# Optimization experiments

Hardware: AMD Instinct MI355X
Metric: run time of the kernel (lower is better)

The kernel has to match this reference:

```python
import math
import jax, jax.numpy as jnp
import numpy as np

HIDDEN = 2048
N_HEAD = 16
HEAD_DIM = HIDDEN // N_HEAD
LAYER_NUMBER = 1  # max(1, layer_number)
NORM_FACTOR = math.sqrt(HEAD_DIM) * LAYER_NUMBER


def build_alibi(seq_len, n_head):
    # n_head is a power of 2 -> slopes_i = 2^(-8*(i+1)/n_head)  (ALiBi paper)
    slopes = 2.0 ** (-8.0 * jnp.arange(1, n_head + 1, dtype=jnp.float32) / n_head)
    pos = jnp.arange(seq_len, dtype=jnp.float32)
    return slopes[:, None, None] * pos[None, None, :]  # (n_head, 1, seq_len)


def setup_inputs() -> dict:
    key = jax.random.key(0)
    ks = jax.random.split(key, 6)
    B, S = 2, 2048
    hidden_states = jax.random.normal(ks[0], (B, S, HIDDEN), jnp.float32)
    residual = jax.random.normal(ks[1], (B, S, HIDDEN), jnp.float32)
    attention_mask = jnp.ones((B, S), jnp.float32)  # no padding
    W_qkv = jax.random.normal(ks[2], (3 * HIDDEN, HIDDEN), jnp.float32) * (1.0 / math.sqrt(HIDDEN))
    b_qkv = jax.random.normal(ks[3], (3 * HIDDEN,), jnp.float32) * 0.02
    W_dense = jax.random.normal(ks[4], (HIDDEN, HIDDEN), jnp.float32) * (1.0 / math.sqrt(HIDDEN))
    b_dense = jax.random.normal(ks[5], (HIDDEN,), jnp.float32) * 0.02
    return {"hidden_states": hidden_states, "residual": residual,
            "attention_mask": attention_mask, "W_qkv": W_qkv, "b_qkv": b_qkv,
            "W_dense": W_dense, "b_dense": b_dense}


def reference(hidden_states, residual, attention_mask, W_qkv, b_qkv, W_dense, b_dense):
    B, S, H = hidden_states.shape
    nh, hd = N_HEAD, HEAD_DIM

    # fused QKV projection; split_tensor_along_last_dim over the per-head 3*hd axis
    mixed = hidden_states @ W_qkv.T + b_qkv              # [B,S,3H]
    mixed = mixed.reshape(B, S, nh, 3, hd)
    q = mixed[..., 0, :]                                  # [B,S,nh,hd]
    k = mixed[..., 1, :]
    v = mixed[..., 2, :]

    # baddbmm: beta*alibi + alpha*(q @ k^T)
    alibi = build_alibi(S, nh)                            # (nh,1,S)
    beta = 1.0 / LAYER_NUMBER
    alpha = 1.0 / NORM_FACTOR
    scores = alpha * jnp.einsum('bqnd,bknd->bnqk', q, k) + beta * alibi[None]  # [B,nh,S,S]

    # BloomScaledSoftmax: scale by layer_number, apply padded causal mask,
    # softmax in fp32, zero out masked probs
    scores = scores * LAYER_NUMBER
    mask_bool = attention_mask == 0.0                     # [B,S] True where padded
    causal = jnp.tril(jnp.ones((S, S), dtype=bool))       # [S,S]
    padded = (mask_bool[:, None, :, None]                 # query side
              | (~causal)[None, None]                     # causal
              | mask_bool[:, None, None, :])              # key side -> [B,1,S,S]
    scores = jnp.where(padded, jnp.float32(-10000.0), scores)
    probs = jax.nn.softmax(scores.astype(jnp.float32), axis=-1) * (~padded)
    probs = probs.astype(v.dtype)

    # attention_dropout/hidden_dropout are identity in eval mode
    context = jnp.einsum('bnqk,bknd->bqnd', probs, v).reshape(B, S, H)
    out = context @ W_dense.T + b_dense                   # dense (skip_bias_add folded)
    return residual + out
```

## Files before the change

### kernel.cpp

```cpp
#include <hip/hip_runtime.h>
#include <math.h>

#define HIDDEN 2048
#define NHEAD 16
#define HD 128
#define SEQ 2048
#define BATCH 2
#define MROWS (BATCH * SEQ)
#define K3 (3 * HIDDEN)

#define SCORE_SCALE 0.08838834764831845f

using short8 = __attribute__((ext_vector_type(8))) short;
using f32x4 = __attribute__((ext_vector_type(4))) float;

__device__ __forceinline__ unsigned short f2bf(float f) {
  union { float f; unsigned int u; } v; v.f = f;
  const unsigned int u = v.u;
  return (unsigned short)((u + 0x7FFFu + ((u >> 16) & 1u)) >> 16);
}

__device__ __forceinline__ void gl2lds16(const void* g, void* l) {
#pragma clang diagnostic push
#pragma clang diagnostic ignored "-Waddress-space-conversion"
  __builtin_amdgcn_global_load_lds(
      (const __attribute__((address_space(1))) unsigned int*)g,
      (__attribute__((address_space(3))) unsigned int*)l, 16, 0, 0);
#pragma clang diagnostic pop
}

template <int N>
__device__ __forceinline__ void vmwait() {
  asm volatile("s_waitcnt vmcnt(%0)" ::"n"(N) : "memory");
}

template <int V> struct IC { static constexpr int v = V; };
template <bool V> struct BC { static constexpr bool v = V; };

__global__ __launch_bounds__(256) void cvt_all(
    const float* __restrict__ s0, unsigned short* __restrict__ d0, int n0,
    const float* __restrict__ s1, unsigned short* __restrict__ d1, int n1,
    const float* __restrict__ s2, unsigned short* __restrict__ d2, int n2) {
  int i = (blockIdx.x * 256 + threadIdx.x) * 8;
  const float* src;
  unsigned short* dst;
  if (i < n0) {
    src = s0; dst = d0;
  } else if (i < n0 + n1) {
    src = s1; dst = d1; i -= n0;
  } else {
    src = s2; dst = d2; i -= n0 + n1;
    if (i >= n2) return;
  }
  const float4 a = *(const float4*)(src + i);
  const float4 b = *(const float4*)(src + i + 4);
  ushort4 oa, ob;
  oa.x = f2bf(a.x); oa.y = f2bf(a.y); oa.z = f2bf(a.z); oa.w = f2bf(a.w);
  ob.x = f2bf(b.x); ob.y = f2bf(b.y); ob.z = f2bf(b.z); ob.w = f2bf(b.w);
  *(ushort4*)(dst + i) = oa;
  *(ushort4*)(dst + i + 4) = ob;
}

template <int MODE, int BROWS>
__global__ __launch_bounds__(512, 2) void gemm256(
    const unsigned short* __restrict__ A, const unsigned short* __restrict__ W,
    const float* __restrict__ bias, const float* __restrict__ residual,
    unsigned short* __restrict__ q, unsigned short* __restrict__ k,
    unsigned short* __restrict__ v, float* __restrict__ outf) {
  constexpr int K = HIDDEN;
  constexpr int NT = K / 64;
  constexpr int NB = BROWS / 64;
  constexpr int ABUF = 32768;
  constexpr int AUNIT = 16384;
  constexpr int BTB = BROWS * 128;
  constexpr int BUNIT = BTB / 2;
  constexpr int LA = 2;
  constexpr int LB = BROWS / 128;
  constexpr int WA = LA + LB;
  __shared__ __align__(16) unsigned short L[(2 * ABUF + 2 * BTB) / 2];

  const int tid = threadIdx.x;
  const int lane = tid & 63;
  const int l15 = lane & 15;
  const int quad = (lane >> 4) & 3;
  const int wave = tid >> 6;
  const int wr = wave >> 2;
  const int wc = wave & 3;

  const int gx = gridDim.x;
  const int nwg = gx * gridDim.y;
  const int flat = blockIdx.y * gx + blockIdx.x;
  const int swz = (flat & 7) * (nwg >> 3) + (flat >> 3);
  const int bx = swz % gx, by = swz / gx;
  const int n0 = bx * BROWS;
  const int m0 = by << 8;

  f32x4 acc[8][NB];
#pragma unroll
  for (int i = 0; i < 8; ++i)
#pragma unroll
    for (int j = 0; j < NB; ++j) {
      f32x4 z = {0.f, 0.f, 0.f, 0.f};
      acc[i][j] = z;
    }

  auto stageAk = [&](const int t, const int buf, const int kk) {
#pragma unroll
    for (int p = 0; p < LA; ++p) {
      const int idx = tid + p * 512;
      gl2lds16(A + (size_t)(m0 + (idx & 255)) * K + t * 64 + kk * 32 +
                   (idx >> 8) * 8,
               (char*)L + buf * ABUF + kk * AUNIT + idx * 16);
    }
  };
  auto stageBk = [&](const int t, const int buf, const int kk) {
#pragma unroll
    for (int p = 0; p < LB; ++p) {
      const int idx = tid + p * 512;
      gl2lds16(W + (size_t)(n0 + (idx & (BROWS - 1))) * K + t * 64 + kk * 32 +
                   (idx / BROWS) * 8,
               (char*)L + 2 * ABUF + buf * BTB + kk * BUNIT + idx * 16);
    }
  };

  short8 afA[4], afB[4], bf0[NB], bf1[NB];

  auto readA = [&](short8 (&dst)[4], const char* lA, const int kk,
                   const int mh) {
#pragma unroll
    for (int i = 0; i < 4; ++i)
      dst[i] = *(const short8*)(
          lA + kk * AUNIT +
          ((quad * 256 + wr * 128 + mh * 64 + i * 16 + l15) << 4));
  };
  auto readB = [&](short8 (&dst)[NB], const char* lB, const int kk) {
#pragma unroll
    for (int j = 0; j < NB; ++j)
      dst[j] = *(const short8*)(
          lB + kk * BUNIT +
          ((quad * BROWS + wc * (BROWS / 4) + j * 16 + l15) << 4));
  };
  auto mfmaC = [&](auto mhc, short8 (&af)[4], short8 (&bf)[NB]) {
    constexpr int MH = decltype(mhc)::v;
    __builtin_amdgcn_s_setprio(1);
#pragma unroll
    for (int i = 0; i < 4; ++i)
#pragma unroll
      for (int j = 0; j < NB; ++j)
        acc[MH + i][j] = __builtin_amdgcn_mfma_f32_16x16x32_bf16(
            af[i], bf[j], acc[MH + i][j], 0, 0, 0);
    __builtin_amdgcn_s_setprio(0);
    __builtin_amdgcn_sched_barrier(0);
  };

  auto tile = [&](const int c, const int t, auto s1c, auto s0c, auto r0c,
                  auto wac, auto wbc) {
    constexpr bool S1 = decltype(s1c)::v;
    constexpr bool S0 = decltype(s0c)::v;
    constexpr bool R0 = decltype(r0c)::v;
    const char* lA = (const char*)L + c * ABUF;
    const char* lB = (const char*)L + 2 * ABUF + c * BTB;
    const char* lAn = (const char*)L + (c ^ 1) * ABUF;
    const char* lBn = (const char*)L + 2 * ABUF + (c ^ 1) * BTB;
    vmwait<decltype(wac)::v>();
    __builtin_amdgcn_s_barrier();
    readA(afB, lA, 1, 0);
    readB(bf1, lB, 1);
    if (S1) stageAk(t + 1, c ^ 1, 1);
    __builtin_amdgcn_sched_barrier(0);
    mfmaC(IC<0>{}, afA, bf0);
    readA(afA, lA, 0, 1);
    if (S1) stageBk(t + 1, c ^ 1, 1);
    __builtin_amdgcn_sched_barrier(0);
    mfmaC(IC<0>{}, afB, bf1);
    readA(afB, lA, 1, 1);
    __builtin_amdgcn_sched_barrier(0);
    mfmaC(IC<4>{}, afA, bf0);
    vmwait<decltype(wbc)::v>();
    __builtin_amdgcn_s_barrier();
    if (R0) {
      readA(afA, lAn, 0, 0);
      readB(bf0, lBn, 0);
    }
    if (S0) {
      stageAk(t + 2, c, 0);
      stageBk(t + 2, c, 0);
    }
    __builtin_amdgcn_sched_barrier(0);
    mfmaC(IC<4>{}, afB, bf1);
  };

  stageAk(0, 0, 0);
  stageBk(0, 0, 0);
  stageAk(0, 0, 1);
  stageBk(0, 0, 1);
  stageAk(1, 1, 0);
  stageBk(1, 1, 0);
  vmwait<2 * WA>();
  __builtin_amdgcn_s_barrier();
  readA(afA, (const char*)L, 0, 0);
  readB(bf0, (const char*)L + 2 * ABUF, 0);

#pragma unroll 1
  for (int t = 0; t < NT - 2; ++t)
    tile(t & 1, t, BC<true>{}, BC<true>{}, BC<true>{}, IC<WA>{}, IC<WA>{});
  tile((NT - 2) & 1, NT - 2, BC<true>{}, BC<false>{}, BC<true>{}, IC<WA>{},
       IC<WA>{});
  tile((NT - 1) & 1, NT - 1, BC<false>{}, BC<false>{}, BC<false>{}, IC<0>{},
       IC<0>{});

  if (MODE == 0) {
#pragma unroll
    for (int mi = 0; mi < 8; ++mi) {
#pragma unroll
      for (int nj = 0; nj < NB; ++nj) {
        const int n = n0 + wc * (BROWS / 4) + nj * 16 + l15;
        const float bi = bias[n];
        const int h = n / 384;
        const int rem = n - h * 384;
        const int which = rem >> 7;
        const int d = rem & 127;
        const int mb = m0 + wr * 128 + mi * 16 + quad * 4;
        const int bb = mb >> 11, ssb = mb & 2047;
        const int bh = (bb << 4) + h;
        if (which == 2) {
          const int dt = d >> 4, dl = d & 15;
          const int ksup = ssb >> 5, ntl = (ssb >> 4) & 1, qq = (ssb >> 2) & 3;
          ushort4 pk;
          pk.x = f2bf(acc[mi][nj][0] + bi);
          pk.y = f2bf(acc[mi][nj][1] + bi);
          pk.z = f2bf(acc[mi][nj][2] + bi);
          pk.w = f2bf(acc[mi][nj][3] + bi);
          *(ushort4*)(v +
                      ((((size_t)(bh * 8 + dt) * (SEQ / 32) + ksup) * 4 + qq) *
                       16 + dl) * 8 + ntl * 4) = pk;
        } else {
          unsigned short* dst = (which == 0) ? q : k;
#pragma unroll
          for (int p = 0; p < 4; ++p)
            dst[((size_t)(bh << 11) + ssb + p) * HD + d] =
                f2bf(acc[mi][nj][p] + bi);
        }
      }
    }
  } else {
#pragma unroll
    for (int mi = 0; mi < 8; ++mi) {
#pragma unroll
      for (int nj = 0; nj < NB; ++nj) {
        const int n = n0 + wc * (BROWS / 4) + nj * 16 + l15;
        const float bi = bias[n];
#pragma unroll
        for (int p = 0; p < 4; ++p) {
          const int m = m0 + wr * 128 + mi * 16 + quad * 4 + p;
          outf[(size_t)m * HIDDEN + n] =
              acc[mi][nj][p] + bi + residual[(size_t)m * HIDDEN + n];
        }
      }
    }
  }
}

__global__ __launch_bounds__(256) void attn_mfma3(
    const unsigned short* __restrict__ qb, const unsigned short* __restrict__ kb,
    const unsigned short* __restrict__ vt4, unsigned short* __restrict__ ctx) {
  __shared__ __align__(16) unsigned short Ks[8192];
  __shared__ __align__(16) unsigned short Vs[8192];

  const int tid = threadIdx.x;
  const int lane = tid & 63;
  const int w = tid >> 6;
  const int l15 = lane & 15;
  const int quad = lane >> 4;
  const int bt = gridDim.x - 1 - blockIdx.x;
  const int q0 = bt << 6;
  const int h = blockIdx.y, b = blockIdx.z;
  const int bh = b * NHEAD + h;
  const float slope = exp2f(-0.5f * (float)(h + 1));
  const unsigned short* qp = qb + ((size_t)bh * SEQ + q0 + w * 16) * HD;
  const unsigned short* kp = kb + (size_t)bh * SEQ * HD;
  const unsigned short* vp = vt4 + (size_t)bh * SEQ * HD;

  short8 qf[4];
#pragma unroll
  for (int dt = 0; dt < 4; ++dt)
    qf[dt] = *(const short8*)(qp + (size_t)l15 * HD + dt * 32 + quad * 8);

  f32x4 O[8];
#pragma unroll
  for (int i = 0; i < 8; ++i) {
    f32x4 z = {0.f, 0.f, 0.f, 0.f};
    O[i] = z;
  }
  float mrow = -3.0e38f, lrow = 0.f;
  const int qg = q0 + w * 16 + l15;

  for (int kt = 0; kt <= bt; ++kt) {
#pragma unroll
    for (int p = 0; p < 4; ++p) {
      const int idx = tid + p * 256;
      const int reg = idx >> 6;
      const int nts = reg >> 2, dts = reg & 3;
      const int qs = (idx >> 4) & 3, ls = idx & 15;
      gl2lds16(kp + (size_t)(kt * 64 + nts * 16 + ls) * HD + dts * 32 + qs * 8,
               (char*)Ks + idx * 16);
    }
#pragma unroll
    for (int p = 0; p < 4; ++p) {
      const int idx = tid + p * 256;
      const int ntv = idx >> 7, off = idx & 127;
      gl2lds16(vp + ((size_t)(ntv * 64 + kt * 2)) * 512 + off * 8,
               (char*)Vs + idx * 16);
    }
    __syncthreads();

    f32x4 sc[4];
#pragma unroll
    for (int nt = 0; nt < 4; ++nt) {
      f32x4 z = {0.f, 0.f, 0.f, 0.f};
      sc[nt] = z;
    }
    const int ntmax = (kt == bt) ? (w + 1) : 4;
#pragma unroll
    for (int dt = 0; dt < 4; ++dt) {
#pragma unroll
      for (int nt = 0; nt < 4; ++nt) {
        if (nt < ntmax) {
          const short8 kf = *(const short8*)(
              (const char*)Ks + ((((nt * 4 + dt) * 4 + quad) * 16 + l15) << 4));
          sc[nt] = __builtin_amdgcn_mfma_f32_16x16x32_bf16(kf, qf[dt], sc[nt],
                                                           0, 0, 0);
        }
      }
    }

    const bool diag = (kt == bt);
    float pv[4][4];
    float pm = -3.0e38f;
#pragma unroll
    for (int nt = 0; nt < 4; ++nt) {
      const int kbase = kt * 64 + nt * 16 + quad * 4;
#pragma unroll
      for (int r = 0; r < 4; ++r) {
        const int kg = kbase + r;
        float s = fmaf(sc[nt][r], SCORE_SCALE, slope * (float)kg);
        if (diag && kg > qg) s = -1.0e30f;
        pv[nt][r] = s;
        pm = fmaxf(pm, s);
      }
    }
    pm = fmaxf(pm, __shfl_xor(pm, 16, 64));
    pm = fmaxf(pm, __shfl_xor(pm, 32, 64));
    const float mnew = fmaxf(mrow, pm);
    const float alpha = __expf(mrow - mnew);
    mrow = mnew;
    float rsum = 0.f;
#pragma unroll
    for (int nt = 0; nt < 4; ++nt)
#pragma unroll
      for (int r = 0; r < 4; ++r) {
        const float p = __expf(pv[nt][r] - mnew);
        pv[nt][r] = p;
        rsum += p;
      }
    rsum += __shfl_xor(rsum, 16, 64);
    rsum += __shfl_xor(rsum, 32, 64);
    lrow = lrow * alpha + rsum;

    float aO[4];
#pragma unroll
    for (int r = 0; r < 4; ++r)
      aO[r] = __shfl(alpha, (quad << 4) + (quad << 2) + r, 64);
#pragma unroll
    for (int o = 0; o < 8; ++o)
#pragma unroll
      for (int r = 0; r < 4; ++r) O[o][r] *= aO[r];

    union { short8 s; unsigned int u[4]; } pf[2];
#pragma unroll
    for (int nt = 0; nt < 4; ++nt) {
      const unsigned int lo =
          (unsigned int)f2bf(pv[nt][0]) | ((unsigned int)f2bf(pv[nt][1]) << 16);
      const unsigned int hi =
          (unsigned int)f2bf(pv[nt][2]) | ((unsigned int)f2bf(pv[nt][3]) << 16);
      pf[nt >> 1].u[(nt & 1) * 2] = lo;
      pf[nt >> 1].u[(nt & 1) * 2 + 1] = hi;
    }

#pragma unroll
    for (int s2 = 0; s2 < 2; ++s2) {
#pragma unroll
      for (int nt = 0; nt < 8; ++nt) {
        const short8 vf = *(const short8*)(
            (const char*)Vs + nt * 2048 + s2 * 1024 + quad * 256 + l15 * 16);
        O[nt] = __builtin_amdgcn_mfma_f32_16x16x32_bf16(pf[s2].s, vf, O[nt],
                                                        0, 0, 0);
      }
    }
    __syncthreads();
  }

  const float linv = 1.f / lrow;
  float iO[4];
#pragma unroll
  for (int r = 0; r < 4; ++r)
    iO[r] = __shfl(linv, (quad << 4) + (quad << 2) + r, 64);
#pragma unroll
  for (int nt = 0; nt < 8; ++nt)
#pragma unroll
    for (int r = 0; r < 4; ++r)
      ctx[((size_t)b * SEQ + q0 + w * 16 + quad * 4 + r) * HIDDEN + h * HD +
          nt * 16 + l15] = f2bf(O[nt][r] * iO[r]);
}

extern "C" void kernel_launch(void* const* d_in, const int* in_sizes, int n_in,
                              void* d_out, int out_size, void* d_ws,
                              size_t ws_size, hipStream_t stream) {
  const float* hs = (const float*)d_in[0];
  const float* res = (const float*)d_in[1];
  const float* Wqkv = (const float*)d_in[3];
  const float* bqkv = (const float*)d_in[4];
  const float* Wd = (const float*)d_in[5];
  const float* bd = (const float*)d_in[6];
  float* out = (float*)d_out;

  const size_t per = (size_t)BATCH * NHEAD * SEQ * HD;
  const size_t n_hs = (size_t)MROWS * HIDDEN;
  const size_t n_wq = (size_t)K3 * HIDDEN;
  const size_t n_wd = (size_t)HIDDEN * HIDDEN;

  unsigned short* ws = (unsigned short*)d_ws;
  unsigned short* qb = ws;
  unsigned short* kb = qb + per;
  unsigned short* vtb = kb + per;
  unsigned short* ctxb = vtb + per;
  unsigned short* hs_bf = ctxb + n_hs;
  unsigned short* wq_bf = hs_bf + n_hs;
  unsigned short* wd_bf = wq_bf + n_wq;

  dim3 blk(256);
  const unsigned cvt_blocks = (unsigned)((n_hs + n_wq + n_wd) / 8 / 256);
  cvt_all<<<dim3(cvt_blocks), blk, 0, stream>>>(
      hs, hs_bf, (int)n_hs, Wqkv, wq_bf, (int)n_wq, Wd, wd_bf, (int)n_wd);
  gemm256<0, 256><<<dim3(K3 / 256, MROWS / 256), dim3(512), 0, stream>>>(
      hs_bf, wq_bf, bqkv, nullptr, qb, kb, vtb, nullptr);
  attn_mfma3<<<dim3(SEQ / 64, NHEAD, BATCH), blk, 0, stream>>>(qb, kb, vtb,
                                                               ctxb);
  gemm256<1, 128><<<dim3(HIDDEN / 128, MROWS / 256), dim3(512), 0, stream>>>(
      ctxb, wd_bf, bd, res, nullptr, nullptr, nullptr, out);
}
```

Before: 565.0 us.

## Stage GEMM tiles through registers instead of direct global-to-LDS loads

Replaces the global_load_lds direct-to-shared staging in the 256-row GEMM with register prefetch: each tile is loaded with coalesced 16-byte global loads into registers two tiles ahead, then written to the alternate LDS buffer after the MFMAs. Synchronisation moves from vmcnt waits and two barriers per tile to one lgkmcnt wait plus barrier. This aims for more contiguous row-wise global reads and a simpler schedule, at the cost of extra VGPRs for staging and explicit LDS stores, which may hurt occupancy under launch_bounds(512,2).

Result: slower. 591.8 us (+4.8%).

```diff
diff --git a/kernel.cpp b/kernel.cpp
--- a/kernel.cpp
+++ b/kernel.cpp
@@ -29,13 +29,7 @@
 #pragma clang diagnostic pop
 }
 
-template <int N>
-__device__ __forceinline__ void vmwait() {
-  asm volatile("s_waitcnt vmcnt(%0)" ::"n"(N) : "memory");
-}
-
 template <int V> struct IC { static constexpr int v = V; };
-template <bool V> struct BC { static constexpr bool v = V; };
 
 __global__ __launch_bounds__(256) void cvt_all(
     const float* __restrict__ s0, unsigned short* __restrict__ d0, int n0,
@@ -74,9 +68,8 @@
   constexpr int AUNIT = 16384;
   constexpr int BTB = BROWS * 128;
   constexpr int BUNIT = BTB / 2;
-  constexpr int LA = 2;
-  constexpr int LB = BROWS / 128;
-  constexpr int WA = LA + LB;
+  constexpr int LAW = 4;
+  constexpr int LBW = BROWS / 64;
   __shared__ __align__(16) unsigned short L[(2 * ABUF + 2 * BTB) / 2];
 
   const int tid = threadIdx.x;
@@ -104,26 +97,38 @@
       acc[i][j] = z;
     }
 
-  auto stageAk = [&](const int t, const int buf, const int kk) {
-#pragma unroll
-    for (int p = 0; p < LA; ++p) {
+  short8 sA[LAW], sB[LBW];
+
+  auto loadG = [&](const int t) {
+#pragma unroll
+    for (int p = 0; p < LAW; ++p) {
       const int idx = tid + p * 512;
-      gl2lds16(A + (size_t)(m0 + (idx & 255)) * K + t * 64 + kk * 32 +
-                   (idx >> 8) * 8,
-               (char*)L + buf * ABUF + kk * AUNIT + idx * 16);
-    }
-  };
-  auto stageBk = [&](const int t, const int buf, const int kk) {
-#pragma unroll
-    for (int p = 0; p < LB; ++p) {
+      sA[p] = *(const short8*)(A + (size_t)(m0 + (idx >> 3)) * K + t * 64 +
+                               (idx & 7) * 8);
+    }
+#pragma unroll
+    for (int p = 0; p < LBW; ++p) {
       const int idx = tid + p * 512;
-      gl2lds16(W + (size_t)(n0 + (idx & (BROWS - 1))) * K + t * 64 + kk * 32 +
-                   (idx / BROWS) * 8,
-               (char*)L + 2 * ABUF + buf * BTB + kk * BUNIT + idx * 16);
-    }
-  };
-
-  short8 afA[4], afB[4], bf0[NB], bf1[NB];
+      sB[p] = *(const short8*)(W + (size_t)(n0 + (idx >> 3)) * K + t * 64 +
+                               (idx & 7) * 8);
+    }
+  };
+  auto writeL = [&](const int buf) {
+#pragma unroll
+    for (int p = 0; p < LAW; ++p) {
+      const int idx = tid + p * 512;
+      const int row = idx >> 3, j = idx & 7;
+      *(short8*)((char*)L + buf * ABUF + (j >> 2) * AUNIT +
+                 (((j & 3) * 256 + row) << 4)) = sA[p];
+    }
+#pragma unroll
+    for (int p = 0; p < LBW; ++p) {
+      const int idx = tid + p * 512;
+      const int row = idx >> 3, j = idx & 7;
+      *(short8*)((char*)L + 2 * ABUF + buf * BTB + (j >> 2) * BUNIT +
+                 (((j & 3) * BROWS + row) << 4)) = sB[p];
+    }
+  };
 
   auto readA = [&](short8 (&dst)[4], const char* lA, const int kk,
                    const int mh) {
@@ -153,61 +158,50 @@
     __builtin_amdgcn_sched_barrier(0);
   };
 
-  auto tile = [&](const int c, const int t, auto s1c, auto s0c, auto r0c,
-                  auto wac, auto wbc) {
-    constexpr bool S1 = decltype(s1c)::v;
-    constexpr bool S0 = decltype(s0c)::v;
-    constexpr bool R0 = decltype(r0c)::v;
+  auto tile_sync = [&] {
+    __builtin_amdgcn_sched_barrier(0);
+    asm volatile("s_waitcnt lgkmcnt(0)" ::: "memory");
+    __builtin_amdgcn_sched_barrier(0);
+    __builtin_amdgcn_s_barrier();
+    __builtin_amdgcn_sched_barrier(0);
+  };
+
+  short8 afA[4], afB[4], bf0[NB], bf1[NB];
+
+  loadG(0);
+  writeL(0);
+  loadG(1);
+  tile_sync();
+  readA(afA, (const char*)L, 0, 0);
+  readB(bf0, (const char*)L + 2 * ABUF, 0);
+
+#pragma unroll 1
+  for (int t = 0; t < NT; ++t) {
+    const int c = t & 1;
     const char* lA = (const char*)L + c * ABUF;
     const char* lB = (const char*)L + 2 * ABUF + c * BTB;
     const char* lAn = (const char*)L + (c ^ 1) * ABUF;
     const char* lBn = (const char*)L + 2 * ABUF + (c ^ 1) * BTB;
-    vmwait<decltype(wac)::v>();
-    __builtin_amdgcn_s_barrier();
     readA(afB, lA, 1, 0);
     readB(bf1, lB, 1);
-    if (S1) stageAk(t + 1, c ^ 1, 1);
     __builtin_amdgcn_sched_barrier(0);
     mfmaC(IC<0>{}, afA, bf0);
     readA(afA, lA, 0, 1);
-    if (S1) stageBk(t + 1, c ^ 1, 1);
     __builtin_amdgcn_sched_barrier(0);
     mfmaC(IC<0>{}, afB, bf1);
     readA(afB, lA, 1, 1);
     __builtin_amdgcn_sched_barrier(0);
     mfmaC(IC<4>{}, afA, bf0);
-    vmwait<decltype(wbc)::v>();
-    __builtin_amdgcn_s_barrier();
-    if (R0) {
+    if (t + 1 < NT) writeL(c ^ 1);
+    if (t + 2 < NT) loadG(t + 2);
+    tile_sync();
+    if (t + 1 < NT) {
       readA(afA, lAn, 0, 0);
       readB(bf0, lBn, 0);
     }
-    if (S0) {
-      stageAk(t + 2, c, 0);
-      stageBk(t + 2, c, 0);
-    }
     __builtin_amdgcn_sched_barrier(0);
     mfmaC(IC<4>{}, afB, bf1);
-  };
-
-  stageAk(0, 0, 0);
-  stageBk(0, 0, 0);
-  stageAk(0, 0, 1);
-  stageBk(0, 0, 1);
-  stageAk(1, 1, 0);
-  stageBk(1, 1, 0);
-  vmwait<2 * WA>();
-  __builtin_amdgcn_s_barrier();
-  readA(afA, (const char*)L, 0, 0);
-  readB(bf0, (const char*)L + 2 * ABUF, 0);
-
-#pragma unroll 1
-  for (int t = 0; t < NT - 2; ++t)
-    tile(t & 1, t, BC<true>{}, BC<true>{}, BC<true>{}, IC<WA>{}, IC<WA>{});
-  tile((NT - 2) & 1, NT - 2, BC<true>{}, BC<false>{}, BC<true>{}, IC<WA>{},
-       IC<WA>{});
-  tile((NT - 1) & 1, NT - 1, BC<false>{}, BC<false>{}, BC<false>{}, IC<0>{},
-       IC<0>{});
+  }
 
   if (MODE == 0) {
 #pragma unroll
```
